# Performance work log

Hardware: AMD Instinct MI355X
Metric: run time of the kernel (lower is better)

## Reference

```python
import jax, jax.numpy as jnp
import numpy as np

M, K, E, N, TOPK = 4096, 1024, 8, 1024, 2

def setup_inputs() -> dict:
    key = jax.random.key(0)
    k1, k2, k3, k4, k5 = jax.random.split(key, 5)
    hidden_states = jax.random.normal(k1, (M, K), dtype=jnp.float32)
    w1 = jax.random.normal(k2, (E, K, 2 * N), dtype=jnp.float32) * 0.02
    w2 = jax.random.normal(k3, (E, N, K), dtype=jnp.float32) * 0.02
    topk_weights = jax.random.uniform(k4, (M, TOPK), dtype=jnp.float32)
    topk_ids = jax.random.randint(k5, (M, TOPK), 0, E, dtype=jnp.int64)
    return {"hidden_states": hidden_states, "w1": w1, "w2": w2,
            "topk_weights": topk_weights, "topk_ids": topk_ids}

def reference(hidden_states, w1, w2, topk_weights, topk_ids):
    # Fused MoE: per expert e, y_e = silu_and_mul(x @ w1[e]) @ w2[e];
    # output[m] = sum_k topk_weights[m,k] * y_{topk_ids[m,k]}[m]
    num_experts = w1.shape[0]
    n = w2.shape[1]

    def expert_step(acc, inputs):
        w1_e, w2_e, e = inputs
        gate_up = hidden_states @ w1_e            # [M, 2N]
        gate, up = gate_up[:, :n], gate_up[:, n:]
        h = jax.nn.silu(gate) * up                 # [M, N]
        y_e = h @ w2_e                             # [M, K]
        # combined routing weight of expert e per token (scatter-free finalize)
        coef = jnp.sum(jnp.where(topk_ids == e, topk_weights, 0.0), axis=1)  # [M]
        return acc + coef[:, None] * y_e, None

    init = jnp.zeros_like(hidden_states)
    out, _ = jax.lax.scan(expert_step, init,
                          (w1, w2, jnp.arange(num_experts, dtype=topk_ids.dtype)))
    return out
```

## Files before the change

### kernel.cpp

```cpp
#include <hip/hip_runtime.h>


#define M_TOK   4096
#define K_DIM   1024
#define N_DIM   1024
#define E_NUM   8
#define NPAIR   8192
#define BM      64
#define ROWS_CAP 8704
#define NROWBLK 136
#define HBLK    32
#define NK      16

typedef unsigned short u16;
typedef unsigned int   u32;
typedef __attribute__((ext_vector_type(8))) short bf16x8;
typedef __attribute__((ext_vector_type(4))) float f32x4;

#define GPTR(p) ((const __attribute__((address_space(1))) u32*)(const void*)(p))
#define LPTR(p) ((__attribute__((address_space(3))) u32*)(void*)(p))

__device__ __forceinline__ u16 f2bf(float f) {
  union { float f; u32 u; } v; v.f = f;
  u32 r = v.u + 0x7FFFu + ((v.u >> 16) & 1u);
  return (u16)(r >> 16);
}
__device__ __forceinline__ float bf2f(u16 u) {
  union { u32 u; float f; } v; v.u = ((u32)u) << 16;
  return v.f;
}

__device__ __forceinline__ void transpose_body(
    const float* __restrict__ in, u16* __restrict__ out, int R, int Cc,
    int xt, int yt, int zt, float (*lds)[65]) {
  const float* src = in + (size_t)zt * R * Cc;
  u16* dst = out + (size_t)zt * R * Cc;
  int r0 = xt * 64, c0 = yt * 64;
  int t = threadIdx.x;
#pragma unroll
  for (int it = 0; it < 16; ++it) {
    int lin = it * 256 + t;
    int rr = lin >> 6, cc = lin & 63;
    lds[cc][rr] = src[(size_t)(r0 + rr) * Cc + c0 + cc];
  }
  __syncthreads();
#pragma unroll
  for (int it = 0; it < 8; ++it) {
    int lin = it * 512 + t * 2;
    int cc = lin >> 6, rr = lin & 63;
    ushort2 o;
    o.x = f2bf(lds[cc][rr]);
    o.y = f2bf(lds[cc][rr + 1]);
    *(ushort2*)&dst[(size_t)(c0 + cc) * R + r0 + rr] = o;
  }
}

__global__ __launch_bounds__(256) void prep_kernel(
    const float* __restrict__ hs, const float* __restrict__ w1,
    const float* __restrict__ w2, const int* __restrict__ topk_ids,
    u16* __restrict__ hsb, u16* __restrict__ w1t, u16* __restrict__ w2t,
    int* __restrict__ blockhist) {
  __shared__ float tlds[64][65];
  __shared__ int wcnt[4][E_NUM];
  const int b = blockIdx.x, t = threadIdx.x;
  if (b < 4096) {
    int i = b * 256 + t;
    float4 v = ((const float4*)hs)[i];
    ushort4 o;
    o.x = f2bf(v.x); o.y = f2bf(v.y); o.z = f2bf(v.z); o.w = f2bf(v.w);
    ((ushort4*)hsb)[i] = o;
  } else if (b < 8192) {
    int idx = b - 4096;
    transpose_body(w1, w1t, 1024, 2048, idx & 15, (idx >> 4) & 31, idx >> 9, tlds);
  } else if (b < 10240) {
    int idx = b - 8192;
    transpose_body(w2, w2t, 1024, 1024, idx & 15, (idx >> 4) & 15, idx >> 8, tlds);
  } else {
    int blk = b - 10240;
    const int wave = t >> 6, lane = t & 63;
    int e = topk_ids[blk * 256 + t] & 7;
#pragma unroll
    for (int ee = 0; ee < E_NUM; ++ee) {
      unsigned long long m = __ballot(e == ee);
      if (lane == ee) wcnt[wave][ee] = (int)__popcll(m);
    }
    __syncthreads();
    if (t < E_NUM)
      blockhist[blk * E_NUM + t] = wcnt[0][t] + wcnt[1][t] + wcnt[2][t] + wcnt[3][t];
  }
}

__global__ __launch_bounds__(256) void scan_kernel(
    const int* __restrict__ blockhist, int* __restrict__ baseoff,
    int* __restrict__ pair_token, int* __restrict__ block_expert) {
  __shared__ int cnt[E_NUM], off[E_NUM], pad[E_NUM];
  const int t = threadIdx.x;
  if (t < E_NUM) {
    int run = 0;
    for (int b = 0; b < HBLK; ++b) {
      baseoff[b * E_NUM + t] = run;
      run += blockhist[b * E_NUM + t];
    }
    cnt[t] = run;
  }
  __syncthreads();
  if (t == 0) {
    int run = 0, blk = 0;
    for (int e = 0; e < E_NUM; ++e) {
      off[e] = run;
      int padded = ((cnt[e] + BM - 1) / BM) * BM;
      pad[e] = padded;
      for (int b = 0; b < padded / BM; ++b) block_expert[blk++] = e;
      run += padded;
    }
    for (; blk < NROWBLK; ++blk) block_expert[blk] = -1;
  }
  __syncthreads();
  for (int i = t; i < HBLK * E_NUM; i += 256) baseoff[i] += off[i & 7];
  for (int e = 0; e < E_NUM; ++e) {
    int s = off[e] + cnt[e], epos = off[e] + pad[e];
    for (int r = s + t; r < epos; r += 256) pair_token[r] = 0;
  }
}

__global__ __launch_bounds__(256) void assign_kernel(
    const int* __restrict__ topk_ids, const int* __restrict__ baseoff,
    int* __restrict__ pair_token, int* __restrict__ pos_of) {
  __shared__ int wcnt[4][E_NUM], wbase[4][E_NUM];
  const int t = threadIdx.x, wave = t >> 6, lane = t & 63;
  const int p = blockIdx.x * 256 + t;
  const int e = topk_ids[p] & 7;
  int rank = 0;
#pragma unroll
  for (int ee = 0; ee < E_NUM; ++ee) {
    unsigned long long m = __ballot(e == ee);
    if (e == ee) rank = (int)__popcll(m & ((1ull << lane) - 1ull));
    if (lane == ee) wcnt[wave][ee] = (int)__popcll(m);
  }
  __syncthreads();
  if (t < E_NUM) {
    int run = baseoff[blockIdx.x * E_NUM + t];
    for (int w = 0; w < 4; ++w) { wbase[w][t] = run; run += wcnt[w][t]; }
  }
  __syncthreads();
  int pos = wbase[wave][e] + rank;
  pair_token[pos] = p >> 1;
  pos_of[p] = pos;
}

template <bool GATHER, int NB, int MINW>
__global__ __launch_bounds__(256, MINW) void gemm_db(
    const u16* __restrict__ A, const u16* __restrict__ Bt, u16* __restrict__ Out,
    const int* __restrict__ pair_token, const int* __restrict__ block_expert) {
  const int by = blockIdx.x & 7;
  const int rbk = blockIdx.x >> 3;
  const int e = block_expert[rbk];
  if (e < 0) return;
  __shared__ __align__(16) u16 As[2 * 4096];
  __shared__ __align__(16) u16 Bs[2 * NB * 8192];
  const int tid = threadIdx.x;
  const int wave = tid >> 6;
  const int lane = tid & 63;
  const int srow = wave * 8 + (lane >> 3);
  const int kc = ((lane & 7) ^ (srow & 7)) << 3;

  const u16* ap[2];
#pragma unroll
  for (int is = 0; is < 2; ++is) {
    int rt = is * 32 + srow;
    int grow = rbk * BM + rt;
    int arow = GATHER ? pair_token[grow] : grow;
    ap[is] = A + (size_t)arow * K_DIM + kc;
  }
  const u16* bp[NB][4];
  const u16* base_e = Bt + (size_t)e * (NB * N_DIM) * K_DIM;
#pragma unroll
  for (int nb = 0; nb < NB; ++nb)
#pragma unroll
    for (int is = 0; is < 4; ++is) {
      int rt = is * 32 + srow;
      int n = nb * N_DIM + by * 128 + rt;
      bp[nb][is] = base_e + (size_t)n * K_DIM + kc;
    }

  f32x4 acc[NB][4][2];
#pragma unroll
  for (int nb = 0; nb < NB; ++nb)
#pragma unroll
    for (int i = 0; i < 4; ++i)
#pragma unroll
      for (int j = 0; j < 2; ++j) acc[nb][i][j] = f32x4{0.f, 0.f, 0.f, 0.f};

#define STAGE(it, buf)                                                         \
  {                                                                            \
    _Pragma("unroll") for (int is = 0; is < 2; ++is)                           \
      __builtin_amdgcn_global_load_lds(GPTR(ap[is] + (it) * 64),               \
          LPTR(As + (buf) * 4096 + wave * 512 + is * 2048), 16, 0, 0);         \
    _Pragma("unroll") for (int nb = 0; nb < NB; ++nb)                          \
      _Pragma("unroll") for (int is = 0; is < 4; ++is)                         \
        __builtin_amdgcn_global_load_lds(GPTR(bp[nb][is] + (it) * 64),         \
            LPTR(Bs + (buf) * NB * 8192 + nb * 8192 + wave * 512 + is * 2048), \
            16, 0, 0);                                                         \
  }

#define HALF(it, cur)                                                          \
  {                                                                            \
    __syncthreads();                                \
    if ((it) + 1 < NK) STAGE((it) + 1, 1 - (cur));                             \
    _Pragma("unroll") for (int ks = 0; ks < 2; ++ks) {                         \
      const int cq = ks * 4 + (lane >> 4);                                     \
      bf16x8 af[4], bfr[NB][2];                                                \
      _Pragma("unroll") for (int i = 0; i < 4; ++i) {                          \
        int row = i * 16 + (lane & 15);                                        \
        af[i] = *(const bf16x8*)&As[(cur) * 4096 + row * 64 +                  \
                                    ((cq ^ (row & 7)) << 3)];                  \
      }                                                                        \
      _Pragma("unroll") for (int nb = 0; nb < NB; ++nb)                        \
        _Pragma("unroll") for (int j = 0; j < 2; ++j) {                        \
          int n = wave * 32 + j * 16 + (lane & 15);                            \
          bfr[nb][j] = *(const bf16x8*)&Bs[(cur) * NB * 8192 + nb * 8192 +     \
                                           n * 64 + ((cq ^ (n & 7)) << 3)];    \
        }                                                                      \
      _Pragma("unroll") for (int nb = 0; nb < NB; ++nb)                        \
        _Pragma("unroll") for (int i = 0; i < 4; ++i)                          \
          _Pragma("unroll") for (int j = 0; j < 2; ++j)                        \
            acc[nb][i][j] = __builtin_amdgcn_mfma_f32_16x16x32_bf16(           \
                af[i], bfr[nb][j], acc[nb][i][j], 0, 0, 0);                    \
    }                                                                          \
  }

  STAGE(0, 0);
  for (int it = 0; it < NK; it += 2) {
    HALF(it, 0);
    HALF(it + 1, 1);
  }
#undef STAGE
#undef HALF

  const size_t rbase = (size_t)rbk * BM + ((lane >> 4) * 4);
  const int cbase = by * 128 + wave * 32 + (lane & 15);
#pragma unroll
  for (int i = 0; i < 4; ++i)
#pragma unroll
    for (int j = 0; j < 2; ++j)
#pragma unroll
      for (int r = 0; r < 4; ++r) {
        float v;
        if (NB == 2) {
          float g = acc[0][i][j][r], u = acc[1][i][j][r];
          v = g * u / (1.f + __expf(-g));
        } else {
          v = acc[0][i][j][r];
        }
        Out[(rbase + i * 16 + r) * N_DIM + cbase + j * 16] = f2bf(v);
      }
}

__global__ __launch_bounds__(256) void gather_kernel(
    const u16* __restrict__ y, const float* __restrict__ tw,
    const int* __restrict__ pos_of, float* __restrict__ out) {
  int m = blockIdx.x;
  int k = threadIdx.x * 4;
  int p0 = pos_of[m * 2 + 0], p1 = pos_of[m * 2 + 1];
  float w0 = tw[m * 2 + 0], w1 = tw[m * 2 + 1];
  ushort4 y0 = *(const ushort4*)&y[(size_t)p0 * 1024 + k];
  ushort4 y1 = *(const ushort4*)&y[(size_t)p1 * 1024 + k];
  float4 o;
  o.x = w0 * bf2f(y0.x) + w1 * bf2f(y1.x);
  o.y = w0 * bf2f(y0.y) + w1 * bf2f(y1.y);
  o.z = w0 * bf2f(y0.z) + w1 * bf2f(y1.z);
  o.w = w0 * bf2f(y0.w) + w1 * bf2f(y1.w);
  *(float4*)&out[(size_t)m * 1024 + k] = o;
}

extern "C" void kernel_launch(void* const* d_in, const int* in_sizes, int n_in,
                              void* d_out, int out_size, void* d_ws, size_t ws_size,
                              hipStream_t stream) {
  const float* hs = (const float*)d_in[0];
  const float* w1 = (const float*)d_in[1];
  const float* w2 = (const float*)d_in[2];
  const float* tw = (const float*)d_in[3];
  const int* tids = (const int*)d_in[4];
  float* out = (float*)d_out;

  char* ws = (char*)d_ws;
  u16* hsb = (u16*)(ws);
  u16* w1t = (u16*)(ws + (size_t)(8u << 20));
  u16* w2t = (u16*)(ws + (size_t)(40u << 20));
  u16* h   = (u16*)(ws + (size_t)(56u << 20));
  u16* y   = (u16*)(ws + (size_t)(76u << 20));
  int* pair_token   = (int*)(ws + (size_t)(96u << 20));
  int* pos_of       = (int*)(ws + (size_t)(96u << 20) + 64 * 1024);
  int* block_expert = (int*)(ws + (size_t)(96u << 20) + 128 * 1024);
  int* blockhist    = (int*)(ws + (size_t)(96u << 20) + 192 * 1024);
  int* baseoff      = (int*)(ws + (size_t)(96u << 20) + 256 * 1024);

  prep_kernel<<<10240 + HBLK, 256, 0, stream>>>(hs, w1, w2, tids, hsb, w1t, w2t, blockhist);
  scan_kernel<<<1, 256, 0, stream>>>(blockhist, baseoff, pair_token, block_expert);
  assign_kernel<<<HBLK, 256, 0, stream>>>(tids, baseoff, pair_token, pos_of);
  gemm_db<true, 2, 2><<<NROWBLK * 8, 256, 0, stream>>>(hsb, w1t, h, pair_token, block_expert);
  gemm_db<false, 1, 3><<<NROWBLK * 8, 256, 0, stream>>>(h, w2t, y, pair_token, block_expert);
  gather_kernel<<<4096, 256, 0, stream>>>(y, tw, pos_of, out);
}
```

Baseline: 268.1 us.

## Enlarge MoE GEMM tiles to 128 rows with 512-thread blocks

Doubles the row tile from 64 to 128 and switches both grouped GEMMs to 512-thread blocks of 8 waves arranged 2x4. The down-projection now computes a 256-column tile per block instead of 128. This raises arithmetic intensity and cuts redundant weight loads per routed row. In exchange it adds padding rows per expert (the row capacity grows), uses more LDS and registers per block, and launches fewer blocks, which may lower occupancy.

```diff
diff --git a/kernel.cpp b/kernel.cpp
--- a/kernel.cpp
+++ b/kernel.cpp
@@ -6,9 +6,9 @@
 #define N_DIM   1024
 #define E_NUM   8
 #define NPAIR   8192
-#define BM      64
-#define ROWS_CAP 8704
-#define NROWBLK 136
+#define BM      128
+#define ROWS_CAP 9216
+#define NROWBLK 72
 #define HBLK    32
 #define NK      16
 
@@ -148,80 +148,83 @@
   pos_of[p] = pos;
 }
 
-template <bool GATHER, int NB, int MINW>
-__global__ __launch_bounds__(256, MINW) void gemm_db(
+template <bool GATHER, bool SILU, int NBY>
+__global__ __launch_bounds__(512, 2) void gemm_big(
     const u16* __restrict__ A, const u16* __restrict__ Bt, u16* __restrict__ Out,
     const int* __restrict__ pair_token, const int* __restrict__ block_expert) {
-  const int by = blockIdx.x & 7;
-  const int rbk = blockIdx.x >> 3;
+  const int by = blockIdx.x % NBY;
+  const int rbk = blockIdx.x / NBY;
   const int e = block_expert[rbk];
   if (e < 0) return;
-  __shared__ __align__(16) u16 As[2 * 4096];
-  __shared__ __align__(16) u16 Bs[2 * NB * 8192];
+  __shared__ __align__(16) u16 As[2 * 8192];
+  __shared__ __align__(16) u16 Bs[2 * 16384];
   const int tid = threadIdx.x;
-  const int wave = tid >> 6;
+  const int w = tid >> 6;
   const int lane = tid & 63;
-  const int srow = wave * 8 + (lane >> 3);
-  const int kc = ((lane & 7) ^ (srow & 7)) << 3;
+  const int lr = lane >> 3;
+  const int lc = lane & 7;
+
+  const int cb0 = SILU ? by * 128 : by * 256;
+  const int cb1 = SILU ? N_DIM + by * 128 : by * 256 + 128;
 
   const u16* ap[2];
 #pragma unroll
-  for (int is = 0; is < 2; ++is) {
-    int rt = is * 32 + srow;
-    int grow = rbk * BM + rt;
+  for (int inst = 0; inst < 2; ++inst) {
+    int row = w * 16 + inst * 8 + lr;
+    int grow = rbk * BM + row;
     int arow = GATHER ? pair_token[grow] : grow;
-    ap[is] = A + (size_t)arow * K_DIM + kc;
-  }
-  const u16* bp[NB][4];
-  const u16* base_e = Bt + (size_t)e * (NB * N_DIM) * K_DIM;
-#pragma unroll
-  for (int nb = 0; nb < NB; ++nb)
-#pragma unroll
-    for (int is = 0; is < 4; ++is) {
-      int rt = is * 32 + srow;
-      int n = nb * N_DIM + by * 128 + rt;
-      bp[nb][is] = base_e + (size_t)n * K_DIM + kc;
-    }
-
-  f32x4 acc[NB][4][2];
-#pragma unroll
-  for (int nb = 0; nb < NB; ++nb)
+    ap[inst] = A + (size_t)arow * K_DIM + (((lc ^ (row & 7)) << 3));
+  }
+  const u16* bp[4];
+  const u16* base_e = Bt + (size_t)e * (2 * N_DIM) * K_DIM;
+  const u16* base_e2 = SILU ? base_e : Bt + (size_t)e * N_DIM * K_DIM;
+#pragma unroll
+  for (int inst = 0; inst < 4; ++inst) {
+    int br = w * 32 + inst * 8 + lr;
+    int rg = (br < 128) ? (cb0 + br) : (cb1 + (br - 128));
+    bp[inst] = base_e2 + (size_t)rg * K_DIM + ((lc ^ (br & 7)) << 3);
+  }
+
+  f32x4 acc[2][4][2];
+#pragma unroll
+  for (int nb = 0; nb < 2; ++nb)
 #pragma unroll
     for (int i = 0; i < 4; ++i)
 #pragma unroll
       for (int j = 0; j < 2; ++j) acc[nb][i][j] = f32x4{0.f, 0.f, 0.f, 0.f};
+
+  const int wm = (w >> 2) * 64;
+  const int wn = (w & 3) * 32;
 
 #define STAGE(it, buf)                                                         \
   {                                                                            \
-    _Pragma("unroll") for (int is = 0; is < 2; ++is)                           \
-      __builtin_amdgcn_global_load_lds(GPTR(ap[is] + (it) * 64),               \
-          LPTR(As + (buf) * 4096 + wave * 512 + is * 2048), 16, 0, 0);         \
-    _Pragma("unroll") for (int nb = 0; nb < NB; ++nb)                          \
-      _Pragma("unroll") for (int is = 0; is < 4; ++is)                         \
-        __builtin_amdgcn_global_load_lds(GPTR(bp[nb][is] + (it) * 64),         \
-            LPTR(Bs + (buf) * NB * 8192 + nb * 8192 + wave * 512 + is * 2048), \
-            16, 0, 0);                                                         \
+    _Pragma("unroll") for (int inst = 0; inst < 2; ++inst)                     \
+      __builtin_amdgcn_global_load_lds(GPTR(ap[inst] + (it) * 64),             \
+          LPTR(As + (buf) * 8192 + (w * 16 + inst * 8) * 64), 16, 0, 0);       \
+    _Pragma("unroll") for (int inst = 0; inst < 4; ++inst)                     \
+      __builtin_amdgcn_global_load_lds(GPTR(bp[inst] + (it) * 64),             \
+          LPTR(Bs + (buf) * 16384 + (w * 32 + inst * 8) * 64), 16, 0, 0);      \
   }
 
 #define HALF(it, cur)                                                          \
   {                                                                            \
-    __syncthreads();                                \
+    __syncthreads();                     \
     if ((it) + 1 < NK) STAGE((it) + 1, 1 - (cur));                             \
     _Pragma("unroll") for (int ks = 0; ks < 2; ++ks) {                         \
       const int cq = ks * 4 + (lane >> 4);                                     \
-      bf16x8 af[4], bfr[NB][2];                                                \
+      bf16x8 af[4], bfr[2][2];                                                 \
       _Pragma("unroll") for (int i = 0; i < 4; ++i) {                          \
-        int row = i * 16 + (lane & 15);                                        \
-        af[i] = *(const bf16x8*)&As[(cur) * 4096 + row * 64 +                  \
+        int row = wm + i * 16 + (lane & 15);                                   \
+        af[i] = *(const bf16x8*)&As[(cur) * 8192 + row * 64 +                  \
                                     ((cq ^ (row & 7)) << 3)];                  \
       }                                                                        \
-      _Pragma("unroll") for (int nb = 0; nb < NB; ++nb)                        \
+      _Pragma("unroll") for (int nb = 0; nb < 2; ++nb)                         \
         _Pragma("unroll") for (int j = 0; j < 2; ++j) {                        \
-          int n = wave * 32 + j * 16 + (lane & 15);                            \
-          bfr[nb][j] = *(const bf16x8*)&Bs[(cur) * NB * 8192 + nb * 8192 +     \
-                                           n * 64 + ((cq ^ (n & 7)) << 3)];    \
+          int br = nb * 128 + wn + j * 16 + (lane & 15);                       \
+          bfr[nb][j] = *(const bf16x8*)&Bs[(cur) * 16384 + br * 64 +           \
+                                           ((cq ^ (br & 7)) << 3)];            \
         }                                                                      \
-      _Pragma("unroll") for (int nb = 0; nb < NB; ++nb)                        \
+      _Pragma("unroll") for (int nb = 0; nb < 2; ++nb)                         \
         _Pragma("unroll") for (int i = 0; i < 4; ++i)                          \
           _Pragma("unroll") for (int j = 0; j < 2; ++j)                        \
             acc[nb][i][j] = __builtin_amdgcn_mfma_f32_16x16x32_bf16(           \
@@ -237,22 +240,25 @@
 #undef STAGE
 #undef HALF
 
-  const size_t rbase = (size_t)rbk * BM + ((lane >> 4) * 4);
-  const int cbase = by * 128 + wave * 32 + (lane & 15);
+  const size_t rbase = (size_t)rbk * BM + wm + ((lane >> 4) * 4);
 #pragma unroll
   for (int i = 0; i < 4; ++i)
 #pragma unroll
     for (int j = 0; j < 2; ++j)
 #pragma unroll
       for (int r = 0; r < 4; ++r) {
-        float v;
-        if (NB == 2) {
+        size_t row = rbase + i * 16 + r;
+        if (SILU) {
           float g = acc[0][i][j][r], u = acc[1][i][j][r];
-          v = g * u / (1.f + __expf(-g));
+          int col = by * 128 + wn + j * 16 + (lane & 15);
+          Out[row * N_DIM + col] = f2bf(g * u / (1.f + __expf(-g)));
         } else {
-          v = acc[0][i][j][r];
+#pragma unroll
+          for (int nb = 0; nb < 2; ++nb) {
+            int col = by * 256 + nb * 128 + wn + j * 16 + (lane & 15);
+            Out[row * K_DIM + col] = f2bf(acc[nb][i][j][r]);
+          }
         }
-        Out[(rbase + i * 16 + r) * N_DIM + cbase + j * 16] = f2bf(v);
       }
 }
 
@@ -298,7 +304,7 @@
   prep_kernel<<<10240 + HBLK, 256, 0, stream>>>(hs, w1, w2, tids, hsb, w1t, w2t, blockhist);
   scan_kernel<<<1, 256, 0, stream>>>(blockhist, baseoff, pair_token, block_expert);
   assign_kernel<<<HBLK, 256, 0, stream>>>(tids, baseoff, pair_token, pos_of);
-  gemm_db<true, 2, 2><<<NROWBLK * 8, 256, 0, stream>>>(hsb, w1t, h, pair_token, block_expert);
-  gemm_db<false, 1, 3><<<NROWBLK * 8, 256, 0, stream>>>(h, w2t, y, pair_token, block_expert);
+  gemm_big<true, true, 8><<<NROWBLK * 8, 512, 0, stream>>>(hsb, w1t, h, pair_token, block_expert);
+  gemm_big<false, false, 4><<<NROWBLK * 4, 512, 0, stream>>>(h, w2t, y, pair_token, block_expert);
   gather_kernel<<<4096, 256, 0, stream>>>(y, tw, pos_of, out);
 }
```

Result: slower. 289.2 us (+7.8%).
